# Kernel tuning notes

Hardware: AMD Instinct MI355X
Metric: run time of the kernel (lower is better)

Reference implementation:

```python
import jax, jax.numpy as jnp
import numpy as np

N = 100000
E = 3200000
F_IN = 128
H1, H2 = 32, 16
R = 8
G = 512  # number of graphs in batch


def setup_inputs() -> dict:
    key = jax.random.key(0)
    ks = jax.random.split(key, 12)
    x = jax.random.normal(ks[0], (N, F_IN), dtype=jnp.float32)
    edge_index = jax.random.randint(ks[1], (2, E), 0, N, dtype=jnp.int64)
    edge_attr = jax.random.randint(ks[2], (E,), 0, R, dtype=jnp.int64)
    batch = jnp.sort(jax.random.randint(ks[3], (N,), 0, G, dtype=jnp.int64))
    s1 = 1.0 / np.sqrt(F_IN)
    s2 = 1.0 / np.sqrt(H1)
    s3 = 1.0 / np.sqrt(H2)
    W1 = jax.random.uniform(ks[4], (R, F_IN, H1), jnp.float32, -s1, s1)
    root1 = jax.random.uniform(ks[5], (F_IN, H1), jnp.float32, -s1, s1)
    b1 = jnp.zeros((H1,), jnp.float32)
    W2 = jax.random.uniform(ks[6], (R, H1, H2), jnp.float32, -s2, s2)
    root2 = jax.random.uniform(ks[7], (H1, H2), jnp.float32, -s2, s2)
    b2 = jnp.zeros((H2,), jnp.float32)
    dense_w = jax.random.uniform(ks[8], (H2, 1), jnp.float32, -s3, s3)
    dense_b = jax.random.uniform(ks[9], (1,), jnp.float32, -s3, s3)
    return dict(x=x, edge_index=edge_index, edge_attr=edge_attr, batch=batch,
                W1=W1, root1=root1, b1=b1, W2=W2, root2=root2, b2=b2,
                dense_w=dense_w, dense_b=dense_b)


def rgcn_layer(x, W, root, b, src, dst, rel, num_rel):
    # Per-relation transform of all nodes: [N, R, out]
    xw = jnp.einsum('ni,rio->nro', x, W)
    msgs = xw[src, rel]                      # gather per edge: [E, out]
    seg = dst * num_rel + rel                # (node, relation) segment id
    nr = x.shape[0] * num_rel
    sums = jax.ops.segment_sum(msgs, seg, num_segments=nr)
    cnt = jax.ops.segment_sum(jnp.ones(src.shape, x.dtype), seg, num_segments=nr)
    mean = sums / jnp.maximum(cnt, 1.0)[:, None]
    agg = mean.reshape(x.shape[0], num_rel, -1).sum(axis=1)  # sum over relations
    return agg + x @ root + b


def reference(x, edge_index, edge_attr, batch, W1, root1, b1, W2, root2, b2, dense_w, dense_b):
    src, dst = edge_index[0], edge_index[1]
    rel = edge_attr
    h = jax.nn.relu(rgcn_layer(x, W1, root1, b1, src, dst, rel, R))
    # F.dropout is treated as identity (inference) for a deterministic reference
    h = jax.nn.relu(rgcn_layer(h, W2, root2, b2, src, dst, rel, R))
    pooled = jax.ops.segment_max(h, batch, num_segments=G)
    pooled = jnp.where(jnp.isfinite(pooled), pooled, 0.0)  # empty graphs -> 0
    return pooled @ dense_w + dense_b
```

## Files before the change

### kernel.cpp

```cpp
#include <hip/hip_runtime.h>
#include <hip/hip_bf16.h>

#define RNUM 8
#define HH1 32
#define HH2 16
#define FIN 128
#define BNODES 256
#define NBMAX 512
#define PCHUNK 8192
#define SORTCAP 11264

#define W1STR 136
#define W1ELTS (288 * W1STR)
#define W2STR 40
#define W2ELTS (144 * W2STR)

typedef short bf16x8 __attribute__((ext_vector_type(8)));
typedef float f32x4 __attribute__((ext_vector_type(4)));

__device__ inline bf16x8 cvt8(const float* __restrict__ p) {
  float tmp[8];
  *(float4*)tmp = *(const float4*)p;
  *(float4*)(tmp + 4) = *(const float4*)(p + 4);
  bf16x8 r;
  #pragma unroll
  for (int j = 0; j < 8; ++j) {
    union { __hip_bfloat16 h; short s; } cv;
    cv.h = __float2bfloat16(tmp[j]);
    r[j] = cv.s;
  }
  return r;
}

__device__ inline bf16x8 cvt8relu(const float* __restrict__ p) {
  float tmp[8];
  *(float4*)tmp = *(const float4*)p;
  *(float4*)(tmp + 4) = *(const float4*)(p + 4);
  bf16x8 r;
  #pragma unroll
  for (int j = 0; j < 8; ++j) {
    union { __hip_bfloat16 h; short s; } cv;
    cv.h = __float2bfloat16(fmaxf(tmp[j], 0.f));
    r[j] = cv.s;
  }
  return r;
}

__device__ inline uint2 pack4bf(f32x4 v) {
  union { unsigned short u[4]; uint2 w; } pk;
  union { __hip_bfloat16 h; unsigned short s; } cv;
  cv.h = __float2bfloat16(v[0]); pk.u[0] = cv.s;
  cv.h = __float2bfloat16(v[1]); pk.u[1] = cv.s;
  cv.h = __float2bfloat16(v[2]); pk.u[2] = cv.s;
  cv.h = __float2bfloat16(v[3]); pk.u[3] = cv.s;
  return pk.w;
}

__global__ __launch_bounds__(256) void k_bhist(const int* __restrict__ ei,
    int* __restrict__ ghist, int E, int NB) {
  __shared__ int h[NBMAX];
  int t = threadIdx.x;
  for (int i = t; i < NBMAX; i += 256) h[i] = 0;
  __syncthreads();
  int base = blockIdx.x * 4096;
  #pragma unroll
  for (int j = 0; j < 16; ++j) {
    int e = base + j * 256 + t;
    if (e < E) atomicAdd(&h[ei[E + e] >> 8], 1);
  }
  __syncthreads();
  for (int i = t; i < NB; i += 256)
    if (h[i]) atomicAdd(&ghist[i], h[i]);
}

__global__ __launch_bounds__(NBMAX) void k_bscan(const int* __restrict__ ghist,
    int* __restrict__ bbase, int* __restrict__ gcursor, int NB, int E) {
  __shared__ int buf[NBMAX];
  int t = threadIdx.x;
  int v = (t < NB) ? ghist[t] : 0;
  buf[t] = v;
  __syncthreads();
  for (int d = 1; d < NBMAX; d <<= 1) {
    int w = (t >= d) ? buf[t - d] : 0;
    __syncthreads();
    buf[t] += w;
    __syncthreads();
  }
  if (t < NB) {
    int ex = buf[t] - v;
    bbase[t] = ex;
    gcursor[t] = ex;
  }
  if (t == 0) bbase[NB] = E;
}

__global__ __launch_bounds__(512) void k_part(const int* __restrict__ ei,
    const int* __restrict__ ea, int* __restrict__ gcursor,
    unsigned* __restrict__ ebuf, int E, int NB) {
  __shared__ unsigned reorder[PCHUNK];
  __shared__ unsigned short bkt[PCHUNK];
  __shared__ int hist[NBMAX], startl[NBMAX], cursor[NBMAX], gb[NBMAX], scanb[NBMAX];
  int t = threadIdx.x;
  int base = blockIdx.x * PCHUNK;
  int cn = min(PCHUNK, E - base);
  unsigned key[16];
  short bb[16];
  hist[t] = 0;
  __syncthreads();
  #pragma unroll
  for (int j = 0; j < 16; ++j) {
    int e = base + j * 512 + t;
    bb[j] = -1;
    if (e < E) {
      int src = ei[e], dst = ei[E + e], rel = ea[e];
      key[j] = ((unsigned)(dst & (BNODES - 1)) << 20) | ((unsigned)src << 3) | (unsigned)rel;
      int b = dst >> 8;
      bb[j] = (short)b;
      atomicAdd(&hist[b], 1);
    }
  }
  __syncthreads();
  int v = hist[t];
  scanb[t] = v;
  __syncthreads();
  for (int d = 1; d < NBMAX; d <<= 1) {
    int w = (t >= d) ? scanb[t - d] : 0;
    __syncthreads();
    scanb[t] += w;
    __syncthreads();
  }
  startl[t] = scanb[t] - v;
  cursor[t] = scanb[t] - v;
  __syncthreads();
  #pragma unroll
  for (int j = 0; j < 16; ++j) {
    if (bb[j] >= 0) {
      int pos = atomicAdd(&cursor[bb[j]], 1);
      reorder[pos] = key[j];
      bkt[pos] = (unsigned short)bb[j];
    }
  }
  __syncthreads();
  if (t < NB && hist[t] > 0) gb[t] = atomicAdd(&gcursor[t], hist[t]);
  __syncthreads();
  for (int p = t; p < cn; p += 512) {
    int b = bkt[p];
    ebuf[gb[b] + (p - startl[b])] = reorder[p];
  }
}

__global__ __launch_bounds__(512) void k_sort(const int* __restrict__ bbase,
    const unsigned* __restrict__ ebuf, unsigned* __restrict__ ebuf2,
    float* __restrict__ wbuf, int* __restrict__ rps, int* __restrict__ rpc,
    int NB) {
  __shared__ int hist[2048];
  __shared__ float invw[2048];
  __shared__ int dlc[256];
  __shared__ unsigned sorted[SORTCAP];
  int t = threadIdx.x;
  int b = blockIdx.x;
  int s = bbase[b], e = bbase[b + 1];
  int out_s = ((s + 7) & ~7) + (b << 11);
  for (int i = t; i < 2048; i += 512) hist[i] = 0;
  __syncthreads();
  for (int p = s + t; p < e; p += 512) {
    unsigned k = ebuf[p];
    atomicAdd(&hist[((k >> 20) << 3) | (k & 7u)], 1);
  }
  __syncthreads();
  for (int i = t; i < 2048; i += 512) {
    int c = hist[i];
    invw[i] = 1.0f / (float)(c > 1 ? c : 1);
  }
  __syncthreads();
  int pr[8];
  int cdl = 0, pc = 0;
  if (t < 256) {
    #pragma unroll
    for (int r = 0; r < 8; ++r) { pr[r] = cdl; cdl += hist[8 * t + r]; }
    pc = (cdl + 7) & ~7;
    dlc[t] = pc;
  }
  __syncthreads();
  for (int d = 1; d < 256; d <<= 1) {
    int w = (t < 256 && t >= d) ? dlc[t - d] : 0;
    __syncthreads();
    if (t < 256) dlc[t] += w;
    __syncthreads();
  }
  if (t < 256) {
    int ebase = dlc[t] - pc;
    #pragma unroll
    for (int r = 0; r < 8; ++r) hist[8 * t + r] = ebase + pr[r];
    rps[(b << 8) + t] = out_s + ebase;
    rpc[(b << 8) + t] = cdl;
  }
  __syncthreads();
  int ptot = dlc[255];
  if (ptot <= SORTCAP) {
    for (int p = t; p < ptot; p += 512) sorted[p] = 0xFFFFFFFFu;
    __syncthreads();
    for (int p = s + t; p < e; p += 512) {
      unsigned k = ebuf[p];
      int pos = atomicAdd(&hist[((k >> 20) << 3) | (k & 7u)], 1);
      sorted[pos] = k;
    }
    __syncthreads();
    for (int p = t; p < ptot; p += 512) {
      unsigned k = sorted[p];
      int o = out_s + p;
      if (k == 0xFFFFFFFFu) { ebuf2[o] = 0u; wbuf[o] = 0.f; }
      else { ebuf2[o] = k; wbuf[o] = invw[((k >> 20) << 3) | (k & 7u)]; }
    }
  } else {
    if (t < 256) {
      int ebase = dlc[t] - pc;
      for (int p = ebase + cdl; p < dlc[t]; ++p) {
        ebuf2[out_s + p] = 0u; wbuf[out_s + p] = 0.f;
      }
    }
    __syncthreads();
    for (int p = s + t; p < e; p += 512) {
      unsigned k = ebuf[p];
      int bin = ((k >> 20) << 3) | (k & 7u);
      int pos = atomicAdd(&hist[bin], 1);
      ebuf2[out_s + pos] = k;
      wbuf[out_s + pos] = invw[bin];
    }
  }
}

__global__ __launch_bounds__(256) void k_prepw(const float* __restrict__ W1,
    const float* __restrict__ root1, const float* __restrict__ W2,
    const float* __restrict__ root2, unsigned short* __restrict__ Wcat,
    unsigned short* __restrict__ W2cat) {
  int id = blockIdx.x * 256 + threadIdx.x;
  union { __hip_bfloat16 h; unsigned short u; } cv;
  if (id < W1ELTS) {
    int c = id / W1STR, kk = id - c * W1STR;
    float v = 0.f;
    if (kk < FIN)
      v = (c < 256) ? W1[((size_t)(c >> 5) * FIN + kk) * HH1 + (c & 31)]
                    : root1[(size_t)kk * HH1 + (c - 256)];
    cv.h = __float2bfloat16(v);
    Wcat[id] = cv.u;
  } else if (id < W1ELTS + W2ELTS) {
    int id2 = id - W1ELTS;
    int c = id2 / W2STR, kk = id2 - c * W2STR;
    float v = 0.f;
    if (kk < HH1)
      v = (c < 128) ? W2[((size_t)(c >> 4) * HH1 + kk) * HH2 + (c & 15)]
                    : root2[(size_t)kk * HH2 + (c - 128)];
    cv.h = __float2bfloat16(v);
    W2cat[id2] = cv.u;
  }
}

__global__ __launch_bounds__(384) void k_gemm1m(const float* __restrict__ x,
    const unsigned short* __restrict__ Wcat, const float* __restrict__ b1,
    __hip_bfloat16* __restrict__ xw, float* __restrict__ agg, int N, int nchunk) {
  int lane = threadIdx.x & 63;
  int wv = threadIdx.x >> 6;
  int g = lane >> 4, lc = lane & 15;
  int cj0 = wv * 3;
  bf16x8 Wf[3][4];
  #pragma unroll
  for (int j = 0; j < 3; ++j)
    #pragma unroll
    for (int ks = 0; ks < 4; ++ks)
      Wf[j][ks] = *(const bf16x8*)(Wcat + (size_t)((cj0 + j) * 16 + lc) * W1STR + ks * 32 + g * 8);

  for (int ch = blockIdx.x; ch < nchunk; ch += gridDim.x) {
    long base = (long)ch * 32;
    long r0 = base + lc;       if (r0 > N - 1) r0 = N - 1;
    long r1 = base + 16 + lc;  if (r1 > N - 1) r1 = N - 1;
    bf16x8 xf0[4], xf1[4];
    #pragma unroll
    for (int ks = 0; ks < 4; ++ks) xf0[ks] = cvt8(x + r0 * FIN + ks * 32 + g * 8);
    #pragma unroll
    for (int ks = 0; ks < 4; ++ks) xf1[ks] = cvt8(x + r1 * FIN + ks * 32 + g * 8);
    f32x4 acc0[3], acc1[3];
    #pragma unroll
    for (int j = 0; j < 3; ++j) {
      acc0[j] = (f32x4){0.f, 0.f, 0.f, 0.f};
      acc1[j] = (f32x4){0.f, 0.f, 0.f, 0.f};
    }
    #pragma unroll
    for (int j = 0; j < 3; ++j)
      #pragma unroll
      for (int ks = 0; ks < 4; ++ks) {
        acc0[j] = __builtin_amdgcn_mfma_f32_16x16x32_bf16(Wf[j][ks], xf0[ks], acc0[j], 0, 0, 0);
        acc1[j] = __builtin_amdgcn_mfma_f32_16x16x32_bf16(Wf[j][ks], xf1[ks], acc1[j], 0, 0, 0);
      }
    long row0 = base + lc;
    if (row0 < N) {
      #pragma unroll
      for (int j = 0; j < 3; ++j) {
        int c0 = (cj0 + j) * 16 + 4 * g;
        if (c0 < 256) {
          *(uint2*)((unsigned short*)xw + row0 * 256 + c0) = pack4bf(acc0[j]);
        } else {
          float4 bb = *(const float4*)(b1 + (c0 - 256));
          float4 o = make_float4(acc0[j][0] + bb.x, acc0[j][1] + bb.y,
                                 acc0[j][2] + bb.z, acc0[j][3] + bb.w);
          *(float4*)(agg + row0 * HH1 + (c0 - 256)) = o;
        }
      }
    }
    long row1 = base + 16 + lc;
    if (row1 < N) {
      #pragma unroll
      for (int j = 0; j < 3; ++j) {
        int c0 = (cj0 + j) * 16 + 4 * g;
        if (c0 < 256) {
          *(uint2*)((unsigned short*)xw + row1 * 256 + c0) = pack4bf(acc1[j]);
        } else {
          float4 bb = *(const float4*)(b1 + (c0 - 256));
          float4 o = make_float4(acc1[j][0] + bb.x, acc1[j][1] + bb.y,
                                 acc1[j][2] + bb.z, acc1[j][3] + bb.w);
          *(float4*)(agg + row1 * HH1 + (c0 - 256)) = o;
        }
      }
    }
  }
}

__global__ __launch_bounds__(256) void k_agg1(const int* __restrict__ rps,
    const int* __restrict__ rpc, const unsigned* __restrict__ eb,
    const float* __restrict__ wb, const __hip_bfloat16* __restrict__ xw,
    float* __restrict__ agg, int N) {
  int d = blockIdx.x * 4 + (threadIdx.x >> 6);
  if (d >= N) return;
  int lane = threadIdx.x & 63;
  int h = lane & 31, half = lane >> 5;
  int s = rps[d];
  int cnt = rpc[d];
  float acc = 0.f;
  for (int j = half * 8; j < cnt; j += 16) {
    const unsigned* kp = eb + s + j;
    uint4 ka = *(const uint4*)kp;
    uint4 kb = *(const uint4*)(kp + 4);
    float4 wa = *(const float4*)(wb + s + j);
    float4 wc = *(const float4*)(wb + s + j + 4);
    unsigned ks[8] = {ka.x, ka.y, ka.z, ka.w, kb.x, kb.y, kb.z, kb.w};
    float ws[8] = {wa.x, wa.y, wa.z, wa.w, wc.x, wc.y, wc.z, wc.w};
    #pragma unroll
    for (int u = 0; u < 8; ++u) {
      unsigned idx = ks[u] & 0xFFFFFu;
      float v = __bfloat162float(xw[((size_t)idx << 5) + h]);
      acc = fmaf(ws[u], v, acc);
    }
  }
  acc += __shfl_xor(acc, 32);
  if (half == 0) agg[((size_t)d << 5) + h] += acc;
}

__global__ __launch_bounds__(256) void k_gemm2m(const float* __restrict__ agg1,
    const unsigned short* __restrict__ W2cat, const float* __restrict__ b2,
    __hip_bfloat16* __restrict__ xw, float* __restrict__ agg, int N) {
  __shared__ short WL[W2ELTS];
  int t = threadIdx.x;
  for (int i = t; i < W2ELTS / 8; i += 256)
    ((uint4*)WL)[i] = ((const uint4*)W2cat)[i];
  __syncthreads();
  int lane = t & 63;
  int wv = t >> 6;
  int g = lane >> 4, lc = lane & 15;
  long nb = (long)blockIdx.x * 128 + wv * 32;
  f32x4 acc[2][9];
  #pragma unroll
  for (int m = 0; m < 2; ++m)
    #pragma unroll
    for (int j = 0; j < 9; ++j)
      acc[m][j] = (f32x4){0.f, 0.f, 0.f, 0.f};
  long rowA0 = nb + lc;       if (rowA0 > N - 1) rowA0 = N - 1;
  long rowA1 = nb + 16 + lc;  if (rowA1 > N - 1) rowA1 = N - 1;
  bf16x8 a0 = cvt8relu(agg1 + rowA0 * HH1 + g * 8);
  bf16x8 a1 = cvt8relu(agg1 + rowA1 * HH1 + g * 8);
  #pragma unroll
  for (int j = 0; j < 9; ++j) {
    bf16x8 bf = *(const bf16x8*)(WL + (16 * j + lc) * W2STR + g * 8);
    acc[0][j] = __builtin_amdgcn_mfma_f32_16x16x32_bf16(bf, a0, acc[0][j], 0, 0, 0);
    acc[1][j] = __builtin_amdgcn_mfma_f32_16x16x32_bf16(bf, a1, acc[1][j], 0, 0, 0);
  }
  #pragma unroll
  for (int m = 0; m < 2; ++m) {
    long row = nb + 16 * m + lc;
    if (row < N) {
      #pragma unroll
      for (int j = 0; j < 8; ++j)
        *(uint2*)((unsigned short*)xw + row * 128 + 16 * j + 4 * g) = pack4bf(acc[m][j]);
      float4 bb = *(const float4*)(b2 + 4 * g);
      float4 o = make_float4(acc[m][8][0] + bb.x, acc[m][8][1] + bb.y,
                             acc[m][8][2] + bb.z, acc[m][8][3] + bb.w);
      *(float4*)(agg + row * HH2 + 4 * g) = o;
    }
  }
}

__global__ __launch_bounds__(256) void k_agg2(const int* __restrict__ rps,
    const int* __restrict__ rpc, const unsigned* __restrict__ eb,
    const float* __restrict__ wb, const __hip_bfloat16* __restrict__ xw,
    float* __restrict__ agg, int N) {
  int d = blockIdx.x * 4 + (threadIdx.x >> 6);
  if (d >= N) return;
  int lane = threadIdx.x & 63;
  int h = lane & 15, q = lane >> 4;
  int s = rps[d];
  int cnt = rpc[d];
  float acc = 0.f;
  for (int j = q * 8; j < cnt; j += 32) {
    const unsigned* kp = eb + s + j;
    uint4 ka = *(const uint4*)kp;
    uint4 kb = *(const uint4*)(kp + 4);
    float4 wa = *(const float4*)(wb + s + j);
    float4 wc = *(const float4*)(wb + s + j + 4);
    unsigned ks[8] = {ka.x, ka.y, ka.z, ka.w, kb.x, kb.y, kb.z, kb.w};
    float ws[8] = {wa.x, wa.y, wa.z, wa.w, wc.x, wc.y, wc.z, wc.w};
    #pragma unroll
    for (int u = 0; u < 8; ++u) {
      unsigned idx = ks[u] & 0xFFFFFu;
      float v = __bfloat162float(xw[((size_t)idx << 4) + h]);
      acc = fmaf(ws[u], v, acc);
    }
  }
  acc += __shfl_xor(acc, 32);
  acc += __shfl_xor(acc, 16);
  if (q == 0) agg[((size_t)d << 4) + h] += acc;
}

__global__ __launch_bounds__(256) void k_pool(const float* __restrict__ agg2,
    const int* __restrict__ batch, unsigned* __restrict__ pooled, int N) {
  int gid = blockIdx.x * 256 + threadIdx.x;
  int n = gid >> 4;
  if (n < N) {
    int h = gid & 15;
    float v = fmaxf(agg2[(size_t)n * HH2 + h], 0.f);
    atomicMax(&pooled[batch[n] * HH2 + h], __float_as_uint(v));
  }
}

__global__ __launch_bounds__(256) void k_dense(const float* __restrict__ pooled,
    const float* __restrict__ dw, const float* __restrict__ db,
    float* __restrict__ out, int Gn) {
  int g = blockIdx.x * 256 + threadIdx.x;
  if (g < Gn) {
    float s = db[0];
    #pragma unroll
    for (int h = 0; h < HH2; ++h) s += pooled[(size_t)g * HH2 + h] * dw[h];
    out[g] = s;
  }
}

extern "C" void kernel_launch(void* const* d_in, const int* in_sizes, int n_in,
                              void* d_out, int out_size, void* d_ws, size_t ws_size,
                              hipStream_t stream) {
  const float* x     = (const float*)d_in[0];
  const int*   ei    = (const int*)d_in[1];
  const int*   ea    = (const int*)d_in[2];
  const int*   batch = (const int*)d_in[3];
  const float* W1    = (const float*)d_in[4];
  const float* root1 = (const float*)d_in[5];
  const float* b1    = (const float*)d_in[6];
  const float* W2    = (const float*)d_in[7];
  const float* root2 = (const float*)d_in[8];
  const float* b2    = (const float*)d_in[9];
  const float* dw    = (const float*)d_in[10];
  const float* db    = (const float*)d_in[11];
  float* out = (float*)d_out;

  const int N  = in_sizes[0] / FIN;
  const int E  = in_sizes[2];
  const int Gn = out_size;
  const int NB = (N + BNODES - 1) / BNODES;

  char* ws = (char*)d_ws;
  size_t off = 0;
  auto walloc = [&](size_t bytes) -> void* {
    void* p = (void*)(ws + off);
    off += (bytes + 255) & ~(size_t)255;
    return p;
  };
  const size_t EP = (size_t)E + (size_t)NBMAX * 2048 + 64;
  int*            ghist   = (int*)            walloc((size_t)NBMAX * 4);
  int*            bbase   = (int*)            walloc(((size_t)NBMAX + 1) * 4);
  int*            gcursor = (int*)            walloc((size_t)NBMAX * 4);
  unsigned*       ebuf    = (unsigned*)       walloc((size_t)E * 4);
  unsigned*       ebuf2   = (unsigned*)       walloc(EP * 4);
  float*          wbuf    = (float*)          walloc(EP * 4);
  int*            rps     = (int*)            walloc((size_t)NBMAX * 256 * 4);
  int*            rpc     = (int*)            walloc((size_t)NBMAX * 256 * 4);
  unsigned short* Wcat    = (unsigned short*) walloc((size_t)W1ELTS * 2);
  unsigned short* W2cat   = (unsigned short*) walloc((size_t)W2ELTS * 2);
  __hip_bfloat16* xw1     = (__hip_bfloat16*) walloc((size_t)N * RNUM * HH1 * 2);
  float*          agg1    = (float*)          walloc((size_t)N * HH1 * 4);
  __hip_bfloat16* xw2     = (__hip_bfloat16*) walloc((size_t)N * RNUM * HH2 * 2);
  float*          agg2    = (float*)          walloc((size_t)N * HH2 * 4);
  unsigned*       pooled  = (unsigned*)       walloc((size_t)Gn * HH2 * 4);

  hipMemsetAsync(ghist, 0, (size_t)NBMAX * 4, stream);
  hipMemsetAsync(pooled, 0, (size_t)Gn * HH2 * 4, stream);

  k_prepw<<<(W1ELTS + W2ELTS + 255) / 256, 256, 0, stream>>>(W1, root1, W2, root2, Wcat, W2cat);
  k_bhist<<<(E + 4095) / 4096, 256, 0, stream>>>(ei, ghist, E, NB);
  k_bscan<<<1, NBMAX, 0, stream>>>(ghist, bbase, gcursor, NB, E);
  k_part<<<(E + PCHUNK - 1) / PCHUNK, 512, 0, stream>>>(ei, ea, gcursor, ebuf, E, NB);
  k_sort<<<NB, 512, 0, stream>>>(bbase, ebuf, ebuf2, wbuf, rps, rpc, NB);

  {
    int nchunk = (N + 31) / 32;
    int g1 = nchunk < 512 ? nchunk : 512;
    k_gemm1m<<<g1, 384, 0, stream>>>(x, Wcat, b1, xw1, agg1, N, nchunk);
  }
  k_agg1<<<(N + 3) / 4, 256, 0, stream>>>(rps, rpc, ebuf2, wbuf, xw1, agg1, N);
  k_gemm2m<<<(N + 127) / 128, 256, 0, stream>>>(agg1, W2cat, b2, xw2, agg2, N);
  k_agg2<<<(N + 3) / 4, 256, 0, stream>>>(rps, rpc, ebuf2, wbuf, xw2, agg2, N);
  k_pool<<<(int)(((long)N * HH2 + 255) / 256), 256, 0, stream>>>(agg2, batch, pooled, N);
  k_dense<<<(Gn + 255) / 256, 256, 0, stream>>>((const float*)pooled, dw, db, out, Gn);
}
```

Measured before the change: 297.3 us.

## Fuse layer-2 transform into layer-1 aggregation and pooling into layer-2 aggregation

Merges the first-layer neighbour aggregation with the second-layer per-relation transform. It adds ReLU to the aggregated features and multiplies them by fp32 W2/root2 staged in LDS, in a grid-stride persistent kernel. It also folds ReLU and the segment-max pooling into the second aggregation kernel, and batches the raw x loads in gemm1 before the bf16 conversion. This removes two launches and the round trips of agg1/agg2 through global memory, but the second-layer GEMM now runs as scalar FMAs with shuffles instead of MFMA.

```diff
diff --git a/kernel.cpp b/kernel.cpp
--- a/kernel.cpp
+++ b/kernel.cpp
@@ -12,35 +12,17 @@
 
 #define W1STR 136
 #define W1ELTS (288 * W1STR)
-#define W2STR 40
-#define W2ELTS (144 * W2STR)
 
 typedef short bf16x8 __attribute__((ext_vector_type(8)));
 typedef float f32x4 __attribute__((ext_vector_type(4)));
 
-__device__ inline bf16x8 cvt8(const float* __restrict__ p) {
-  float tmp[8];
-  *(float4*)tmp = *(const float4*)p;
-  *(float4*)(tmp + 4) = *(const float4*)(p + 4);
+__device__ inline bf16x8 cvt8r(float4 a, float4 b) {
+  float tmp[8] = {a.x, a.y, a.z, a.w, b.x, b.y, b.z, b.w};
   bf16x8 r;
   #pragma unroll
   for (int j = 0; j < 8; ++j) {
     union { __hip_bfloat16 h; short s; } cv;
     cv.h = __float2bfloat16(tmp[j]);
-    r[j] = cv.s;
-  }
-  return r;
-}
-
-__device__ inline bf16x8 cvt8relu(const float* __restrict__ p) {
-  float tmp[8];
-  *(float4*)tmp = *(const float4*)p;
-  *(float4*)(tmp + 4) = *(const float4*)(p + 4);
-  bf16x8 r;
-  #pragma unroll
-  for (int j = 0; j < 8; ++j) {
-    union { __hip_bfloat16 h; short s; } cv;
-    cv.h = __float2bfloat16(fmaxf(tmp[j], 0.f));
     r[j] = cv.s;
   }
   return r;
@@ -231,29 +213,17 @@
 }
 
 __global__ __launch_bounds__(256) void k_prepw(const float* __restrict__ W1,
-    const float* __restrict__ root1, const float* __restrict__ W2,
-    const float* __restrict__ root2, unsigned short* __restrict__ Wcat,
-    unsigned short* __restrict__ W2cat) {
+    const float* __restrict__ root1, unsigned short* __restrict__ Wcat) {
   int id = blockIdx.x * 256 + threadIdx.x;
+  if (id >= W1ELTS) return;
   union { __hip_bfloat16 h; unsigned short u; } cv;
-  if (id < W1ELTS) {
-    int c = id / W1STR, kk = id - c * W1STR;
-    float v = 0.f;
-    if (kk < FIN)
-      v = (c < 256) ? W1[((size_t)(c >> 5) * FIN + kk) * HH1 + (c & 31)]
-                    : root1[(size_t)kk * HH1 + (c - 256)];
-    cv.h = __float2bfloat16(v);
-    Wcat[id] = cv.u;
-  } else if (id < W1ELTS + W2ELTS) {
-    int id2 = id - W1ELTS;
-    int c = id2 / W2STR, kk = id2 - c * W2STR;
-    float v = 0.f;
-    if (kk < HH1)
-      v = (c < 128) ? W2[((size_t)(c >> 4) * HH1 + kk) * HH2 + (c & 15)]
-                    : root2[(size_t)kk * HH2 + (c - 128)];
-    cv.h = __float2bfloat16(v);
-    W2cat[id2] = cv.u;
-  }
+  int c = id / W1STR, kk = id - c * W1STR;
+  float v = 0.f;
+  if (kk < FIN)
+    v = (c < 256) ? W1[((size_t)(c >> 5) * FIN + kk) * HH1 + (c & 31)]
+                  : root1[(size_t)kk * HH1 + (c - 256)];
+  cv.h = __float2bfloat16(v);
+  Wcat[id] = cv.u;
 }
 
 __global__ __launch_bounds__(384) void k_gemm1m(const float* __restrict__ x,
@@ -274,11 +244,25 @@
     long base = (long)ch * 32;
     long r0 = base + lc;       if (r0 > N - 1) r0 = N - 1;
     long r1 = base + 16 + lc;  if (r1 > N - 1) r1 = N - 1;
+    const float4* p0 = (const float4*)(x + r0 * FIN + g * 8);
+    const float4* p1 = (const float4*)(x + r1 * FIN + g * 8);
+    float4 raw[16];
+    #pragma unroll
+    for (int ks = 0; ks < 4; ++ks) {
+      raw[2 * ks]     = p0[ks * 8];
+      raw[2 * ks + 1] = p0[ks * 8 + 1];
+    }
+    #pragma unroll
+    for (int ks = 0; ks < 4; ++ks) {
+      raw[8 + 2 * ks]     = p1[ks * 8];
+      raw[8 + 2 * ks + 1] = p1[ks * 8 + 1];
+    }
     bf16x8 xf0[4], xf1[4];
     #pragma unroll
-    for (int ks = 0; ks < 4; ++ks) xf0[ks] = cvt8(x + r0 * FIN + ks * 32 + g * 8);
-    #pragma unroll
-    for (int ks = 0; ks < 4; ++ks) xf1[ks] = cvt8(x + r1 * FIN + ks * 32 + g * 8);
+    for (int ks = 0; ks < 4; ++ks) {
+      xf0[ks] = cvt8r(raw[2 * ks], raw[2 * ks + 1]);
+      xf1[ks] = cvt8r(raw[8 + 2 * ks], raw[8 + 2 * ks + 1]);
+    }
     f32x4 acc0[3], acc1[3];
     #pragma unroll
     for (int j = 0; j < 3; ++j) {
@@ -325,83 +309,72 @@
   }
 }
 
-__global__ __launch_bounds__(256) void k_agg1(const int* __restrict__ rps,
+__global__ __launch_bounds__(256) void k_agg1f(const int* __restrict__ rps,
     const int* __restrict__ rpc, const unsigned* __restrict__ eb,
     const float* __restrict__ wb, const __hip_bfloat16* __restrict__ xw,
-    float* __restrict__ agg, int N) {
-  int d = blockIdx.x * 4 + (threadIdx.x >> 6);
-  if (d >= N) return;
-  int lane = threadIdx.x & 63;
+    const float* __restrict__ agg1r, const float* __restrict__ W2,
+    const float* __restrict__ root2, const float* __restrict__ b2,
+    __hip_bfloat16* __restrict__ xw2, float* __restrict__ agg2r, int N) {
+  __shared__ float WLf[144 * 33];
+  int t = threadIdx.x;
+  for (int i = t; i < 144 * HH1; i += 256) {
+    int c = i >> 5, kk = i & 31;
+    float v = (c < 128) ? W2[((size_t)(c >> 4) * HH1 + kk) * HH2 + (c & 15)]
+                        : root2[(size_t)kk * HH2 + (c - 128)];
+    WLf[c * 33 + kk] = v;
+  }
+  __syncthreads();
+  int lane = t & 63;
   int h = lane & 31, half = lane >> 5;
-  int s = rps[d];
-  int cnt = rpc[d];
-  float acc = 0.f;
-  for (int j = half * 8; j < cnt; j += 16) {
-    const unsigned* kp = eb + s + j;
-    uint4 ka = *(const uint4*)kp;
-    uint4 kb = *(const uint4*)(kp + 4);
-    float4 wa = *(const float4*)(wb + s + j);
-    float4 wc = *(const float4*)(wb + s + j + 4);
-    unsigned ks[8] = {ka.x, ka.y, ka.z, ka.w, kb.x, kb.y, kb.z, kb.w};
-    float ws[8] = {wa.x, wa.y, wa.z, wa.w, wc.x, wc.y, wc.z, wc.w};
-    #pragma unroll
-    for (int u = 0; u < 8; ++u) {
-      unsigned idx = ks[u] & 0xFFFFFu;
-      float v = __bfloat162float(xw[((size_t)idx << 5) + h]);
-      acc = fmaf(ws[u], v, acc);
-    }
-  }
-  acc += __shfl_xor(acc, 32);
-  if (half == 0) agg[((size_t)d << 5) + h] += acc;
-}
-
-__global__ __launch_bounds__(256) void k_gemm2m(const float* __restrict__ agg1,
-    const unsigned short* __restrict__ W2cat, const float* __restrict__ b2,
-    __hip_bfloat16* __restrict__ xw, float* __restrict__ agg, int N) {
-  __shared__ short WL[W2ELTS];
-  int t = threadIdx.x;
-  for (int i = t; i < W2ELTS / 8; i += 256)
-    ((uint4*)WL)[i] = ((const uint4*)W2cat)[i];
-  __syncthreads();
-  int lane = t & 63;
-  int wv = t >> 6;
-  int g = lane >> 4, lc = lane & 15;
-  long nb = (long)blockIdx.x * 128 + wv * 32;
-  f32x4 acc[2][9];
-  #pragma unroll
-  for (int m = 0; m < 2; ++m)
-    #pragma unroll
-    for (int j = 0; j < 9; ++j)
-      acc[m][j] = (f32x4){0.f, 0.f, 0.f, 0.f};
-  long rowA0 = nb + lc;       if (rowA0 > N - 1) rowA0 = N - 1;
-  long rowA1 = nb + 16 + lc;  if (rowA1 > N - 1) rowA1 = N - 1;
-  bf16x8 a0 = cvt8relu(agg1 + rowA0 * HH1 + g * 8);
-  bf16x8 a1 = cvt8relu(agg1 + rowA1 * HH1 + g * 8);
-  #pragma unroll
-  for (int j = 0; j < 9; ++j) {
-    bf16x8 bf = *(const bf16x8*)(WL + (16 * j + lc) * W2STR + g * 8);
-    acc[0][j] = __builtin_amdgcn_mfma_f32_16x16x32_bf16(bf, a0, acc[0][j], 0, 0, 0);
-    acc[1][j] = __builtin_amdgcn_mfma_f32_16x16x32_bf16(bf, a1, acc[1][j], 0, 0, 0);
-  }
-  #pragma unroll
-  for (int m = 0; m < 2; ++m) {
-    long row = nb + 16 * m + lc;
-    if (row < N) {
+  int wid0 = blockIdx.x * 4 + (t >> 6);
+  int stride = gridDim.x * 4;
+  for (int d = wid0; d < N; d += stride) {
+    int s = rps[d];
+    int cnt = rpc[d];
+    float acc = 0.f;
+    for (int j = half * 8; j < cnt; j += 16) {
+      const unsigned* kp = eb + s + j;
+      uint4 ka = *(const uint4*)kp;
+      uint4 kb = *(const uint4*)(kp + 4);
+      float4 wa = *(const float4*)(wb + s + j);
+      float4 wc = *(const float4*)(wb + s + j + 4);
+      unsigned ks[8] = {ka.x, ka.y, ka.z, ka.w, kb.x, kb.y, kb.z, kb.w};
+      float ws[8] = {wa.x, wa.y, wa.z, wa.w, wc.x, wc.y, wc.z, wc.w};
       #pragma unroll
-      for (int j = 0; j < 8; ++j)
-        *(uint2*)((unsigned short*)xw + row * 128 + 16 * j + 4 * g) = pack4bf(acc[m][j]);
-      float4 bb = *(const float4*)(b2 + 4 * g);
-      float4 o = make_float4(acc[m][8][0] + bb.x, acc[m][8][1] + bb.y,
-                             acc[m][8][2] + bb.z, acc[m][8][3] + bb.w);
-      *(float4*)(agg + row * HH2 + 4 * g) = o;
-    }
-  }
-}
-
-__global__ __launch_bounds__(256) void k_agg2(const int* __restrict__ rps,
+      for (int u = 0; u < 8; ++u) {
+        unsigned idx = ks[u] & 0xFFFFFu;
+        float v = __bfloat162float(xw[((size_t)idx << 5) + h]);
+        acc = fmaf(ws[u], v, acc);
+      }
+    }
+    acc += __shfl_xor(acc, 32);
+    float z = fmaxf(agg1r[((size_t)d << 5) + h] + acc, 0.f);
+    float o0 = 0.f, o1 = 0.f, o2 = 0.f;
+    const float* w0 = WLf + lane * 33;
+    const float* w1 = WLf + (lane + 64) * 33;
+    const float* w2c = WLf + (lane + 128) * 33;
+    #pragma unroll 8
+    for (int hh = 0; hh < 32; ++hh) {
+      float zh = __shfl(z, hh);
+      o0 = fmaf(zh, w0[hh], o0);
+      o1 = fmaf(zh, w1[hh], o1);
+      if (lane < 16) o2 = fmaf(zh, w2c[hh], o2);
+    }
+    unsigned short* xo = (unsigned short*)xw2 + ((size_t)d << 7);
+    union { __hip_bfloat16 hh; unsigned short u; } cv;
+    cv.hh = __float2bfloat16(o0);
+    xo[lane] = cv.u;
+    cv.hh = __float2bfloat16(o1);
+    xo[lane + 64] = cv.u;
+    if (lane < 16) agg2r[((size_t)d << 4) + lane] = o2 + b2[lane];
+  }
+}
+
+__global__ __launch_bounds__(256) void k_agg2f(const int* __restrict__ rps,
     const int* __restrict__ rpc, const unsigned* __restrict__ eb,
     const float* __restrict__ wb, const __hip_bfloat16* __restrict__ xw,
-    float* __restrict__ agg, int N) {
+    const float* __restrict__ agg2r, const int* __restrict__ batch,
+    unsigned* __restrict__ pooled, int N) {
   int d = blockIdx.x * 4 + (threadIdx.x >> 6);
   if (d >= N) return;
   int lane = threadIdx.x & 63;
@@ -426,17 +399,9 @@
   }
   acc += __shfl_xor(acc, 32);
   acc += __shfl_xor(acc, 16);
-  if (q == 0) agg[((size_t)d << 4) + h] += acc;
-}
-
-__global__ __launch_bounds__(256) void k_pool(const float* __restrict__ agg2,
-    const int* __restrict__ batch, unsigned* __restrict__ pooled, int N) {
-  int gid = blockIdx.x * 256 + threadIdx.x;
-  int n = gid >> 4;
-  if (n < N) {
-    int h = gid & 15;
-    float v = fmaxf(agg2[(size_t)n * HH2 + h], 0.f);
-    atomicMax(&pooled[batch[n] * HH2 + h], __float_as_uint(v));
+  if (q == 0) {
+    float v = fmaxf(acc + agg2r[((size_t)d << 4) + h], 0.f);
+    atomicMax(&pooled[batch[d] * HH2 + h], __float_as_uint(v));
   }
 }
 
@@ -491,17 +456,16 @@
   int*            rps     = (int*)            walloc((size_t)NBMAX * 256 * 4);
   int*            rpc     = (int*)            walloc((size_t)NBMAX * 256 * 4);
   unsigned short* Wcat    = (unsigned short*) walloc((size_t)W1ELTS * 2);
-  unsigned short* W2cat   = (unsigned short*) walloc((size_t)W2ELTS * 2);
   __hip_bfloat16* xw1     = (__hip_bfloat16*) walloc((size_t)N * RNUM * HH1 * 2);
   float*          agg1    = (float*)          walloc((size_t)N * HH1 * 4);
   __hip_bfloat16* xw2     = (__hip_bfloat16*) walloc((size_t)N * RNUM * HH2 * 2);
-  float*          agg2    = (float*)          walloc((size_t)N * HH2 * 4);
+  float*          agg2r   = (float*)          walloc((size_t)N * HH2 * 4);
   unsigned*       pooled  = (unsigned*)       walloc((size_t)Gn * HH2 * 4);
 
   hipMemsetAsync(ghist, 0, (size_t)NBMAX * 4, stream);
   hipMemsetAsync(pooled, 0, (size_t)Gn * HH2 * 4, stream);
 
-  k_prepw<<<(W1ELTS + W2ELTS + 255) / 256, 256, 0, stream>>>(W1, root1, W2, root2, Wcat, W2cat);
+  k_prepw<<<(W1ELTS + 255) / 256, 256, 0, stream>>>(W1, root1, Wcat);
   k_bhist<<<(E + 4095) / 4096, 256, 0, stream>>>(ei, ghist, E, NB);
   k_bscan<<<1, NBMAX, 0, stream>>>(ghist, bbase, gcursor, NB, E);
   k_part<<<(E + PCHUNK - 1) / PCHUNK, 512, 0, stream>>>(ei, ea, gcursor, ebuf, E, NB);
@@ -512,9 +476,9 @@
     int g1 = nchunk < 512 ? nchunk : 512;
     k_gemm1m<<<g1, 384, 0, stream>>>(x, Wcat, b1, xw1, agg1, N, nchunk);
   }
-  k_agg1<<<(N + 3) / 4, 256, 0, stream>>>(rps, rpc, ebuf2, wbuf, xw1, agg1, N);
-  k_gemm2m<<<(N + 127) / 128, 256, 0, stream>>>(agg1, W2cat, b2, xw2, agg2, N);
-  k_agg2<<<(N + 3) / 4, 256, 0, stream>>>(rps, rpc, ebuf2, wbuf, xw2, agg2, N);
-  k_pool<<<(int)(((long)N * HH2 + 255) / 256), 256, 0, stream>>>(agg2, batch, pooled, N);
+  k_agg1f<<<2048, 256, 0, stream>>>(rps, rpc, ebuf2, wbuf, xw1, agg1,
+                                    W2, root2, b2, xw2, agg2r, N);
+  k_agg2f<<<(N + 3) / 4, 256, 0, stream>>>(rps, rpc, ebuf2, wbuf, xw2,
+                                           agg2r, batch, pooled, N);
   k_dense<<<(Gn + 255) / 256, 256, 0, stream>>>((const float*)pooled, dw, db, out, Gn);
 }
```

Result: faster. 287.7 us (-3.3%).
